# Kernel optimization log

Measured on AMD Instinct MI355X. Metric: run time of the kernel, lower is better.

Reference implementation:

```python
import jax, jax.numpy as jnp
import numpy as np
from jax import lax


def setup_inputs() -> dict:
    key = jax.random.key(0)
    k1, k2, k3, k4 = jax.random.split(key, 4)
    B, K, Hp, Wp = 512, 64, 5, 5
    num_classes = 10
    x = jax.random.uniform(k1, (B, 1, 20, 20), dtype=jnp.float32)
    patterns = jax.random.uniform(k2, (K, 1, Hp, Wp), dtype=jnp.float32)
    w2 = jax.random.normal(k3, (1, K), dtype=jnp.float32) * 0.1
    b2 = jnp.zeros((1,), dtype=jnp.float32)
    wf = jax.random.normal(k4, (num_classes, 400), dtype=jnp.float32) * 0.05
    bf = jnp.zeros((num_classes,), dtype=jnp.float32)
    return {"x": x, "patterns": patterns, "w2": w2, "b2": b2, "wf": wf, "bf": bf}


def _geneo1(patterns, x):
    # patterns: (K,1,Hp,Wp), x: (B,1,H,W). Same-padded sliding L1 similarity.
    K, _, Hp, Wp = patterns.shape
    P = Hp * Wp
    xp = jnp.pad(x, ((0, 0), (0, 0), (Hp // 2, Hp // 2), (Wp // 2, Wp // 2)))
    # (B, P, H_out, W_out); C=1 so feature order is row-major over (Hp,Wp),
    # matching torch's unfold(2,Hp,1).unfold(3,Wp,1).reshape(-1).
    patches = lax.conv_general_dilated_patches(xp, (Hp, Wp), (1, 1), "VALID")
    pat = patterns.reshape(K, P)
    # (B,K,H_out,W_out): mean_|p| |pattern - patch|
    diff = jnp.abs(pat[None, :, :, None, None] - patches[:, None, :, :, :]).mean(axis=2)
    return 1.0 - diff


def _channel_wise_max(t):
    B, K, H, W = t.shape
    flat = t.reshape(B, K, H * W)
    idx = jnp.argmax(flat, axis=2)                      # (B,K)
    mask = jax.nn.one_hot(idx, H * W, dtype=flat.dtype) # (B,K,HW)
    return (flat * mask).reshape(B, K, H, W)


def reference(x, patterns, w2, b2, wf, bf):
    Fk = _geneo1(patterns, x)            # (B,K,20,20)
    cwm = _channel_wise_max(Fk)          # (B,K,20,20)
    # GENEO2: Linear(K,1) over channel dim (applied on (B,H,W,K))
    t = jnp.einsum("bkhw,ok->bhwo", cwm, w2) + b2   # (B,20,20,1)
    t = jax.nn.sigmoid(t)
    out = t.reshape(t.shape[0], -1) @ wf.T + bf      # (B,num_classes)
    return jax.nn.sigmoid(out)
```

## Files before the change

### kernel.cpp

```cpp
#include <hip/hip_runtime.h>
#include <math.h>

#define NB 512
#define NK 64
#define NP 25
#define HW 400
#define NC 10
#define NWAVE 16

__device__ __forceinline__ unsigned sad16(unsigned a, unsigned b, unsigned c) {
#if __has_builtin(__builtin_amdgcn_sad_u16)
    return __builtin_amdgcn_sad_u16(a, b, c);
#else
    unsigned d;
    asm("v_sad_u16 %0, %1, %2, %3" : "=v"(d) : "v"(a), "v"(b), "v"(c));
    return d;
#endif
}

__global__ __launch_bounds__(1024, 4) void geneo_mlp_kernel(
    const float* __restrict__ x,
    const float* __restrict__ patterns,
    const float* __restrict__ w2,
    const float* __restrict__ b2,
    const float* __restrict__ wf,
    const float* __restrict__ bf,
    float* __restrict__ out)
{
    __shared__ unsigned xq[24 * 24];
    __shared__ unsigned pqd[23 * 24];
    __shared__ __align__(16) float pat_lds[NK * NP];
    __shared__ unsigned redbest[NWAVE][NK];
    __shared__ float2 contrib[NK];
    __shared__ float  wsum[NWAVE][NC];

    const int tid  = threadIdx.x;
    const int b    = blockIdx.x;
    const int lane = tid & 63;
    const int wave = tid >> 6;

    if (tid < 576) {
        const int h = tid / 24, w = tid - h * 24;
        float v = 0.f;
        if (h >= 2 && h < 22 && w >= 2 && w < 22)
            v = x[b * HW + (h - 2) * 20 + (w - 2)];
        xq[tid] = (unsigned)(v * 65535.f + 0.5f);
    }
    if (tid < 400)
        reinterpret_cast<float4*>(pat_lds)[tid] =
            reinterpret_cast<const float4*>(patterns)[tid];
    __syncthreads();

    if (tid < 552)
        pqd[tid] = xq[tid] | (xq[tid + 24] << 16);

    unsigned vp01[5], vp23[5], p4v[5];
    #pragma unroll
    for (int c = 0; c < 5; ++c) {
        const unsigned q0 = (unsigned)(pat_lds[lane * NP +  0 + c] * 65535.f + 0.5f);
        const unsigned q1 = (unsigned)(pat_lds[lane * NP +  5 + c] * 65535.f + 0.5f);
        const unsigned q2 = (unsigned)(pat_lds[lane * NP + 10 + c] * 65535.f + 0.5f);
        const unsigned q3 = (unsigned)(pat_lds[lane * NP + 15 + c] * 65535.f + 0.5f);
        const unsigned q4 = (unsigned)(pat_lds[lane * NP + 20 + c] * 65535.f + 0.5f);
        vp01[c] = q0 | (q1 << 16);
        vp23[c] = q2 | (q3 << 16);
        p4v[c]  = q4;
    }
    __syncthreads();

    const int tr = wave >> 2;
    const int tc = wave & 3;
    const int c0 = tc * 5;
    unsigned best = 0xFFFFFFFFu;

    #pragma unroll 1
    for (int r = 0; r < 5; ++r) {
        const int h = tr * 5 + r;
        const unsigned* r01 = &pqd[h * 24 + c0];
        const unsigned* r23 = &pqd[(h + 2) * 24 + c0];
        const unsigned* r4  = &xq[(h + 4) * 24 + c0];
        unsigned W01[9], W23[9], W4[9];
        #pragma unroll
        for (int d = 0; d < 9; ++d) {
            W01[d] = r01[d]; W23[d] = r23[d]; W4[d] = r4[d];
        }
        #pragma unroll
        for (int px = 0; px < 5; ++px) {
            unsigned s = 0;
            #pragma unroll
            for (int dx = 0; dx < 5; ++dx) {
                s = sad16(W01[px + dx], vp01[dx], s);
                s = sad16(W23[px + dx], vp23[dx], s);
                s = sad16(W4 [px + dx], p4v [dx], s);
            }
            const unsigned pk = (s << 9) | (unsigned)(h * 20 + c0 + px);
            best = min(best, pk);
        }
    }
    redbest[wave][lane] = best;
    __syncthreads();

    if (tid < NK) {
        unsigned b0 = redbest[0][tid];
        #pragma unroll
        for (int w = 1; w < NWAVE; ++w) b0 = min(b0, redbest[w][tid]);
        const unsigned s  = b0 >> 9;
        const int    pix  = (int)(b0 & 511u);
        const float  F    = 1.f - (float)s * (1.f / (25.f * 65535.f));
        contrib[tid] = make_float2(F * w2[tid], __int_as_float(pix));
    }
    __syncthreads();

    float acc[NC];
    #pragma unroll
    for (int c = 0; c < NC; ++c) acc[c] = 0.f;

    if (tid < HW) {
        float s = b2[0];
        #pragma unroll 8
        for (int k = 0; k < NK; ++k) {
            const float2 cv = contrib[k];
            if (__float_as_int(cv.y) == tid) s += cv.x;
        }
        const float t = 1.f / (1.f + expf(-s));
        #pragma unroll
        for (int c = 0; c < NC; ++c) acc[c] += t * wf[c * HW + tid];
    }

    #pragma unroll
    for (int c = 0; c < NC; ++c) {
        #pragma unroll
        for (int off = 32; off >= 1; off >>= 1)
            acc[c] += __shfl_down(acc[c], off);
    }
    if (lane == 0) {
        #pragma unroll
        for (int c = 0; c < NC; ++c) wsum[wave][c] = acc[c];
    }
    __syncthreads();
    if (tid < NC) {
        float s = bf[tid];
        #pragma unroll
        for (int w = 0; w < NWAVE; ++w) s += wsum[w][tid];
        out[b * NC + tid] = 1.f / (1.f + expf(-s));
    }
}

extern "C" void kernel_launch(void* const* d_in, const int* in_sizes, int n_in,
                              void* d_out, int out_size, void* d_ws, size_t ws_size,
                              hipStream_t stream) {
    const float* x        = (const float*)d_in[0];
    const float* patterns = (const float*)d_in[1];
    const float* w2       = (const float*)d_in[2];
    const float* b2       = (const float*)d_in[3];
    const float* wf       = (const float*)d_in[4];
    const float* bf       = (const float*)d_in[5];
    float* out = (float*)d_out;

    geneo_mlp_kernel<<<NB, 1024, 0, stream>>>(x, patterns, w2, b2, wf, bf, out);
}
```

Measured before the change: 21.51 us.

## Use shifted LDS copies for vector loads and sparse-delta final projection

The padded image is replicated into four column-shifted LDS copies so that each wave's window loads become aligned 128-bit reads instead of scalar reads. The final layer is rewritten algebraically: a baseline sigmoid(b2) times the column sums of wf, plus sparse corrections only at the at most 64 argmax pixels. This replaces the 400-thread dense pass and its 16-wave reduction. The change adds extra LDS copy passes and a barrier, and relaxes launch bounds from 4 to 1.

```diff
diff --git a/kernel.cpp b/kernel.cpp
--- a/kernel.cpp
+++ b/kernel.cpp
@@ -3,10 +3,8 @@
 
 #define NB 512
 #define NK 64
-#define NP 25
 #define HW 400
 #define NC 10
-#define NWAVE 16
 
 __device__ __forceinline__ unsigned sad16(unsigned a, unsigned b, unsigned c) {
 #if __has_builtin(__builtin_amdgcn_sad_u16)
@@ -18,7 +16,7 @@
 #endif
 }
 
-__global__ __launch_bounds__(1024, 4) void geneo_mlp_kernel(
+__global__ __launch_bounds__(1024, 1) void geneo_mlp_kernel(
     const float* __restrict__ x,
     const float* __restrict__ patterns,
     const float* __restrict__ w2,
@@ -27,12 +25,13 @@
     const float* __restrict__ bf,
     float* __restrict__ out)
 {
-    __shared__ unsigned xq[24 * 24];
-    __shared__ unsigned pqd[23 * 24];
-    __shared__ __align__(16) float pat_lds[NK * NP];
-    __shared__ unsigned redbest[NWAVE][NK];
-    __shared__ float2 contrib[NK];
-    __shared__ float  wsum[NWAVE][NC];
+    __shared__ __align__(16) unsigned xq4[4][576];
+    __shared__ __align__(16) unsigned pqd4[4][552];
+    __shared__ __align__(16) float pat_lds[NK * 25];
+    __shared__ unsigned redbest[16][NK];
+    __shared__ float2 pixcv[NK];
+    __shared__ float colsum[NC];
+    __shared__ float redout[NC];
 
     const int tid  = threadIdx.x;
     const int b    = blockIdx.x;
@@ -44,46 +43,65 @@
         float v = 0.f;
         if (h >= 2 && h < 22 && w >= 2 && w < 22)
             v = x[b * HW + (h - 2) * 20 + (w - 2)];
-        xq[tid] = (unsigned)(v * 65535.f + 0.5f);
+        xq4[0][tid] = (unsigned)(v * 65535.f + 0.5f);
+    } else if (tid < 976) {
+        const int i = tid - 576;
+        reinterpret_cast<float4*>(pat_lds)[i] =
+            reinterpret_cast<const float4*>(patterns)[i];
     }
-    if (tid < 400)
-        reinterpret_cast<float4*>(pat_lds)[tid] =
-            reinterpret_cast<const float4*>(patterns)[tid];
     __syncthreads();
 
-    if (tid < 552)
-        pqd[tid] = xq[tid] | (xq[tid + 24] << 16);
+    for (int i = tid; i < 3 * 576; i += 1024) {
+        const int j = i / 576 + 1;
+        const int w = i - (j - 1) * 576;
+        int src = w + j; if (src > 575) src = 575;
+        xq4[j][w] = xq4[0][src];
+    }
+    __syncthreads();
+
+    for (int i = tid; i < 4 * 552; i += 1024) {
+        const int j = i / 552;
+        const int w = i - j * 552;
+        pqd4[j][w] = xq4[j][w] | (xq4[j][w + 24] << 16);
+    }
 
     unsigned vp01[5], vp23[5], p4v[5];
     #pragma unroll
     for (int c = 0; c < 5; ++c) {
-        const unsigned q0 = (unsigned)(pat_lds[lane * NP +  0 + c] * 65535.f + 0.5f);
-        const unsigned q1 = (unsigned)(pat_lds[lane * NP +  5 + c] * 65535.f + 0.5f);
-        const unsigned q2 = (unsigned)(pat_lds[lane * NP + 10 + c] * 65535.f + 0.5f);
-        const unsigned q3 = (unsigned)(pat_lds[lane * NP + 15 + c] * 65535.f + 0.5f);
-        const unsigned q4 = (unsigned)(pat_lds[lane * NP + 20 + c] * 65535.f + 0.5f);
+        const unsigned q0 = (unsigned)(pat_lds[lane * 25 +  0 + c] * 65535.f + 0.5f);
+        const unsigned q1 = (unsigned)(pat_lds[lane * 25 +  5 + c] * 65535.f + 0.5f);
+        const unsigned q2 = (unsigned)(pat_lds[lane * 25 + 10 + c] * 65535.f + 0.5f);
+        const unsigned q3 = (unsigned)(pat_lds[lane * 25 + 15 + c] * 65535.f + 0.5f);
+        const unsigned q4 = (unsigned)(pat_lds[lane * 25 + 20 + c] * 65535.f + 0.5f);
         vp01[c] = q0 | (q1 << 16);
         vp23[c] = q2 | (q3 << 16);
         p4v[c]  = q4;
     }
     __syncthreads();
 
-    const int tr = wave >> 2;
-    const int tc = wave & 3;
-    const int c0 = tc * 5;
-    unsigned best = 0xFFFFFFFFu;
+    const int tr   = wave >> 2;
+    const int tc   = wave & 3;
+    const int base = 4 * tc;
+    unsigned best  = 0xFFFFFFFFu;
 
     #pragma unroll 1
     for (int r = 0; r < 5; ++r) {
         const int h = tr * 5 + r;
-        const unsigned* r01 = &pqd[h * 24 + c0];
-        const unsigned* r23 = &pqd[(h + 2) * 24 + c0];
-        const unsigned* r4  = &xq[(h + 4) * 24 + c0];
-        unsigned W01[9], W23[9], W4[9];
-        #pragma unroll
-        for (int d = 0; d < 9; ++d) {
-            W01[d] = r01[d]; W23[d] = r23[d]; W4[d] = r4[d];
-        }
+        const unsigned* r01 = &pqd4[tc][h * 24 + base];
+        const unsigned* r23 = &pqd4[tc][(h + 2) * 24 + base];
+        const unsigned* r4  = &xq4[tc][(h + 4) * 24 + base];
+        uint4 A0 = *reinterpret_cast<const uint4*>(r01);
+        uint4 A1 = *reinterpret_cast<const uint4*>(r01 + 4);
+        unsigned A8 = r01[8];
+        uint4 B0 = *reinterpret_cast<const uint4*>(r23);
+        uint4 B1 = *reinterpret_cast<const uint4*>(r23 + 4);
+        unsigned B8 = r23[8];
+        uint4 C0 = *reinterpret_cast<const uint4*>(r4);
+        uint4 C1 = *reinterpret_cast<const uint4*>(r4 + 4);
+        unsigned C8 = r4[8];
+        const unsigned W01[9] = {A0.x, A0.y, A0.z, A0.w, A1.x, A1.y, A1.z, A1.w, A8};
+        const unsigned W23[9] = {B0.x, B0.y, B0.z, B0.w, B1.x, B1.y, B1.z, B1.w, B8};
+        const unsigned W4 [9] = {C0.x, C0.y, C0.z, C0.w, C1.x, C1.y, C1.z, C1.w, C8};
         #pragma unroll
         for (int px = 0; px < 5; ++px) {
             unsigned s = 0;
@@ -93,55 +111,60 @@
                 s = sad16(W23[px + dx], vp23[dx], s);
                 s = sad16(W4 [px + dx], p4v [dx], s);
             }
-            const unsigned pk = (s << 9) | (unsigned)(h * 20 + c0 + px);
+            const unsigned pk = (s << 9) | (unsigned)(h * 20 + tc * 5 + px);
             best = min(best, pk);
         }
     }
     redbest[wave][lane] = best;
     __syncthreads();
 
-    if (tid < NK) {
-        unsigned b0 = redbest[0][tid];
+    if (wave < NC) {
+        float sc = 0.f;
+        for (int p = lane; p < HW; p += 64) sc += wf[wave * HW + p];
         #pragma unroll
-        for (int w = 1; w < NWAVE; ++w) b0 = min(b0, redbest[w][tid]);
-        const unsigned s  = b0 >> 9;
-        const int    pix  = (int)(b0 & 511u);
-        const float  F    = 1.f - (float)s * (1.f / (25.f * 65535.f));
-        contrib[tid] = make_float2(F * w2[tid], __int_as_float(pix));
+        for (int off = 32; off >= 1; off >>= 1) sc += __shfl_down(sc, off);
+        if (lane == 0) colsum[wave] = sc;
+    }
+    if (wave == 15) {
+        unsigned b0 = redbest[0][lane];
+        #pragma unroll
+        for (int w = 1; w < 16; ++w) b0 = min(b0, redbest[w][lane]);
+        const float F  = 1.f - (float)(b0 >> 9) * (1.f / (25.f * 65535.f));
+        const float cv = F * w2[lane];
+        pixcv[lane] = make_float2(cv, __int_as_float((int)(b0 & 511u)));
     }
     __syncthreads();
 
-    float acc[NC];
-    #pragma unroll
-    for (int c = 0; c < NC; ++c) acc[c] = 0.f;
-
-    if (tid < HW) {
-        float s = b2[0];
+    if (wave == 0) {
+        const int mypix = __float_as_int(pixcv[lane].y);
+        float ssum = 0.f;
+        int   firstj = 64;
         #pragma unroll 8
-        for (int k = 0; k < NK; ++k) {
-            const float2 cv = contrib[k];
-            if (__float_as_int(cv.y) == tid) s += cv.x;
+        for (int j = 0; j < NK; ++j) {
+            const float2 pc = pixcv[j];
+            if (__float_as_int(pc.y) == mypix) {
+                ssum += pc.x;
+                if (j < firstj) firstj = j;
+            }
         }
-        const float t = 1.f / (1.f + expf(-s));
+        const float b2v = b2[0];
+        const float t0  = 1.f / (1.f + expf(-b2v));
+        const float t   = 1.f / (1.f + expf(-(b2v + ssum)));
+        const float dlt = (firstj == lane) ? (t - t0) : 0.f;
         #pragma unroll
-        for (int c = 0; c < NC; ++c) acc[c] += t * wf[c * HW + tid];
-    }
-
-    #pragma unroll
-    for (int c = 0; c < NC; ++c) {
-        #pragma unroll
-        for (int off = 32; off >= 1; off >>= 1)
-            acc[c] += __shfl_down(acc[c], off);
-    }
-    if (lane == 0) {
-        #pragma unroll
-        for (int c = 0; c < NC; ++c) wsum[wave][c] = acc[c];
+        for (int c = 0; c < NC; ++c) {
+            float v = dlt * wf[c * HW + mypix];
+            #pragma unroll
+            for (int off = 32; off >= 1; off >>= 1) v += __shfl_down(v, off);
+            if (lane == 0) redout[c] = v;
+        }
     }
     __syncthreads();
+
     if (tid < NC) {
-        float s = bf[tid];
-        #pragma unroll
-        for (int w = 0; w < NWAVE; ++w) s += wsum[w][tid];
+        const float b2v = b2[0];
+        const float t0  = 1.f / (1.f + expf(-b2v));
+        const float s   = t0 * colsum[tid] + redout[tid] + bf[tid];
         out[b * NC + tid] = 1.f / (1.f + expf(-s));
     }
 }
```

Measured after the change: 20.81 us. 3.3% less time.
